# Optimization experiments

Measured on AMD Instinct MI355X. Metric: run time of the kernel, lower is better.

The kernel has to match this reference:

```python
import jax, jax.numpy as jnp
import numpy as np

N_NODES = 50000
N_EDGES = 800000
IN_CH = 128
OUT_CH = 64
HEADS = 2
NEG_SLOPE = 0.2


def _gat_conv(x, src, dst, W, a_src, a_dst, b, n):
    """PyG-style GATConv (eval mode: no dropout), self-loops already appended.
    x: [n, F_in]; W: [F_in, H*C]; a_src/a_dst: [H, C]; b: [H*C]."""
    H, C = a_src.shape
    h = (x @ W).reshape(n, H, C)                       # [n, H, C]
    alpha_src = jnp.sum(h * a_src, axis=-1)            # [n, H]
    alpha_dst = jnp.sum(h * a_dst, axis=-1)            # [n, H]
    e = alpha_src[src] + alpha_dst[dst]                # [E, H]
    e = jnp.where(e > 0, e, NEG_SLOPE * e)             # LeakyReLU(0.2)
    # neighbor-wise (destination-grouped) softmax, numerically stable
    m = jax.ops.segment_max(e, dst, num_segments=n)
    e = jnp.exp(e - m[dst])
    denom = jax.ops.segment_sum(e, dst, num_segments=n)
    alpha = e / (denom[dst] + 1e-16)                   # [E, H]
    out = jax.ops.segment_sum(alpha[:, :, None] * h[src], dst, num_segments=n)
    return out.reshape(n, H * C) + b


def setup_inputs() -> dict:
    key = jax.random.key(0)
    ks = jax.random.split(key, 12)
    s = 0.08  # glorot-ish scale
    x = jax.random.normal(ks[0], (N_NODES, IN_CH), dtype=jnp.float32)
    edge_index = jax.random.randint(ks[1], (2, N_EDGES), 0, N_NODES, dtype=jnp.int64)
    H, O = HEADS, OUT_CH
    return {
        "x": x,
        "edge_index": edge_index,
        "W1": jax.random.normal(ks[2], (IN_CH, H * 2 * O), dtype=jnp.float32) * s,
        "a_src1": jax.random.normal(ks[3], (H, 2 * O), dtype=jnp.float32) * s,
        "a_dst1": jax.random.normal(ks[4], (H, 2 * O), dtype=jnp.float32) * s,
        "b1": jnp.zeros((H * 2 * O,), dtype=jnp.float32),
        "W_mu": jax.random.normal(ks[5], (2 * O * H, H * O), dtype=jnp.float32) * s,
        "a_src_mu": jax.random.normal(ks[6], (H, O), dtype=jnp.float32) * s,
        "a_dst_mu": jax.random.normal(ks[7], (H, O), dtype=jnp.float32) * s,
        "b_mu": jnp.zeros((H * O,), dtype=jnp.float32),
        "W_ls": jax.random.normal(ks[8], (2 * O * H, H * O), dtype=jnp.float32) * s,
        "a_src_ls": jax.random.normal(ks[9], (H, O), dtype=jnp.float32) * s,
        "a_dst_ls": jax.random.normal(ks[10], (H, O), dtype=jnp.float32) * s,
        "b_ls": jnp.zeros((H * O,), dtype=jnp.float32),
    }


def reference(x, edge_index, W1, a_src1, a_dst1, b1,
              W_mu, a_src_mu, a_dst_mu, b_mu,
              W_ls, a_src_ls, a_dst_ls, b_ls):
    n = x.shape[0]
    loop = jnp.arange(n, dtype=edge_index.dtype)
    src = jnp.concatenate([edge_index[0], loop])  # PyG add_self_loops=True
    dst = jnp.concatenate([edge_index[1], loop])
    x1 = jax.nn.elu(_gat_conv(x, src, dst, W1, a_src1, a_dst1, b1, n))
    mu = _gat_conv(x1, src, dst, W_mu, a_src_mu, a_dst_mu, b_mu, n)
    logstd = _gat_conv(x1, src, dst, W_ls, a_src_ls, a_dst_ls, b_ls, n)
    return (mu, logstd)
```

## Files before the change

### kernel.cpp

```cpp
#include <hip/hip_runtime.h>


typedef unsigned short u16;
typedef unsigned int u32;
typedef _Float16 f16;
typedef f16 f16x8 __attribute__((ext_vector_type(8)));
typedef float f32x4v __attribute__((ext_vector_type(4)));

__device__ __forceinline__ u16 f2h(float f) {
    union { f16 h; u16 u; } t;
    t.h = (f16)f;
    return t.u;
}
__device__ __forceinline__ float4 loadh4(const u16* __restrict__ p, size_t i) {
    union { uint2 u; f16 h[4]; } t;
    t.u = *(const uint2*)(p + i);
    return make_float4((float)t.h[0], (float)t.h[1], (float)t.h[2], (float)t.h[3]);
}
__device__ __forceinline__ void store4(float* __restrict__ p, size_t i, float4 v) {
    *(float4*)(p + i) = v;
}
__device__ __forceinline__ void store4(u16* __restrict__ p, size_t i, float4 v) {
    union { uint2 u; f16 h[4]; } t;
    t.h[0] = (f16)v.x; t.h[1] = (f16)v.y; t.h[2] = (f16)v.z; t.h[3] = (f16)v.w;
    *(uint2*)(p + i) = t.u;
}

__global__ __launch_bounds__(256) void k_detect(const u32* __restrict__ ebuf,
                                                int* __restrict__ flag) {
    __shared__ int nz;
    if (threadIdx.x == 0) nz = 0;
    __syncthreads();
    if (ebuf[2 * threadIdx.x + 1] != 0u) atomicAdd(&nz, 1);
    __syncthreads();
    if (threadIdx.x == 0) *flag = (nz == 0) ? 1 : 0;
}

__global__ __launch_bounds__(256) void k_extract(const u32* __restrict__ ebuf, int E,
                                                 const int* __restrict__ flag,
                                                 int* __restrict__ se,
                                                 int* __restrict__ de,
                                                 int* __restrict__ deg) {
    int e = blockIdx.x * 256 + threadIdx.x;
    if (e >= E) return;
    int s, d;
    if (*flag) {
        s = (int)ebuf[2 * (size_t)e];
        d = (int)ebuf[2 * ((size_t)E + (size_t)e)];
    } else {
        s = (int)ebuf[e];
        d = (int)ebuf[(size_t)E + (size_t)e];
    }
    se[e] = s;
    de[e] = d;
    atomicAdd(&deg[d], 1);
}

__global__ __launch_bounds__(256) void k_scan_a(const int* __restrict__ deg, int n,
                                                int* __restrict__ bsum) {
    __shared__ int s[256];
    int i = blockIdx.x * 256 + threadIdx.x;
    s[threadIdx.x] = (i < n) ? deg[i] : 0;
    __syncthreads();
    for (int st = 128; st > 0; st >>= 1) {
        if (threadIdx.x < st) s[threadIdx.x] += s[threadIdx.x + st];
        __syncthreads();
    }
    if (threadIdx.x == 0) bsum[blockIdx.x] = s[0];
}

__global__ __launch_bounds__(256) void k_scan_b(int* __restrict__ bsum, int nb) {
    __shared__ int s[256];
    int t = threadIdx.x;
    int v = (t < nb) ? bsum[t] : 0;
    s[t] = v;
    __syncthreads();
    for (int off = 1; off < 256; off <<= 1) {
        int add = (t >= off) ? s[t - off] : 0;
        __syncthreads();
        s[t] += add;
        __syncthreads();
    }
    if (t < nb) bsum[t] = s[t] - v;
}

__global__ __launch_bounds__(256) void k_scan_c(const int* __restrict__ deg, int n,
                                                const int* __restrict__ bsum,
                                                int* __restrict__ rowptr,
                                                int* __restrict__ cursor, int E) {
    __shared__ int s[256];
    int t = threadIdx.x;
    int i = blockIdx.x * 256 + t;
    int v = (i < n) ? deg[i] : 0;
    s[t] = v;
    __syncthreads();
    for (int off = 1; off < 256; off <<= 1) {
        int add = (t >= off) ? s[t - off] : 0;
        __syncthreads();
        s[t] += add;
        __syncthreads();
    }
    if (i < n) {
        int ex = bsum[blockIdx.x] + s[t] - v;
        rowptr[i] = ex;
        cursor[i] = ex;
    }
    if (i == 0) rowptr[n] = E;
}

__global__ __launch_bounds__(256) void k_fill(const int* __restrict__ src,
                                              const int* __restrict__ dst, int E,
                                              int* __restrict__ cursor,
                                              int* __restrict__ csr_src) {
    int e = blockIdx.x * 256 + threadIdx.x;
    if (e < E) {
        int d = dst[e];
        int slot = atomicAdd(&cursor[d], 1);
        csr_src[slot] = src[e];
    }
}

__global__ __launch_bounds__(256) void k_cvt(const float* __restrict__ in,
                                             u16* __restrict__ out, int nElem) {
    int i = (blockIdx.x * 256 + threadIdx.x) * 4;
    if (i >= nElem) return;
    float4 v = *(const float4*)(in + i);
    store4(out, i, v);
}

__global__ __launch_bounds__(256) void k_tw(const float* __restrict__ Wl,
                                            const float* __restrict__ Wr, int split,
                                            int K, u16* __restrict__ Wt) {
    int idx = blockIdx.x * 256 + threadIdx.x;
    if (idx >= 256 * K) return;
    int c = idx / K, k = idx - c * K;
    float v;
    if (split == 256)
        v = Wl[(size_t)k * 256 + c];
    else
        v = (c < 128) ? Wl[(size_t)k * 128 + c] : Wr[(size_t)k * 128 + (c - 128)];
    Wt[idx] = f2h(v);
}

template <int K, int ALOGW>
__global__ __launch_bounds__(256) void k_gemm_mfma(
    const u16* __restrict__ Ah, const u16* __restrict__ Wt, u16* __restrict__ out,
    float* __restrict__ as_out, float* __restrict__ ad_out,
    const float* __restrict__ alo, const float* __restrict__ ahi,
    const float* __restrict__ dlo, const float* __restrict__ dhi, int M) {
    __shared__ u16 Bs[256 * 40];
    const int tid = threadIdx.x;
    const int wave = tid >> 6;
    const int lane = tid & 63;
    const int li = lane & 15;
    const int quad = lane >> 4;
    const int r0 = blockIdx.x * 64 + wave * 16;
    int arowi = r0 + li;
    if (arowi >= M) arowi = M - 1;
    const u16* arow = Ah + (size_t)arowi * K + quad * 8;

    f32x4v acc[16];
#pragma unroll
    for (int ct = 0; ct < 16; ct++) acc[ct] = (f32x4v)(0.f);

    for (int t = 0; t < K; t += 32) {
        __syncthreads();
        {
            const u16* src = Wt + (size_t)tid * K + t;
            u16* dst = Bs + tid * 40;
            uint4 v0 = ((const uint4*)src)[0];
            uint4 v1 = ((const uint4*)src)[1];
            uint4 v2 = ((const uint4*)src)[2];
            uint4 v3 = ((const uint4*)src)[3];
            ((uint4*)dst)[0] = v0;
            ((uint4*)(dst + 8))[0] = v1;
            ((uint4*)(dst + 16))[0] = v2;
            ((uint4*)(dst + 24))[0] = v3;
        }
        __syncthreads();
        f16x8 a = *(const f16x8*)(arow + t);
#pragma unroll
        for (int ct = 0; ct < 16; ct++) {
            f16x8 b = *(const f16x8*)(Bs + (ct * 16 + li) * 40 + quad * 8);
            acc[ct] = __builtin_amdgcn_mfma_f32_16x16x32_f16(a, b, acc[ct], 0, 0, 0);
        }
    }

#pragma unroll
    for (int reg = 0; reg < 4; reg++) {
        int grow = r0 + quad * 4 + reg;
        if (grow < M) {
            u16* orow = out + (size_t)grow * 256 + li;
#pragma unroll
            for (int ct = 0; ct < 16; ct++) orow[ct * 16] = f2h(acc[ct][reg]);
        }
    }

    const int NS = 64 >> ALOGW;
    const int SH = ALOGW - 2;
    float aw[16], dw[16];
#pragma unroll
    for (int ct = 0; ct < 16; ct++) {
        int col = ct * 16 + li;
        aw[ct] = (col < 128) ? alo[col] : ahi[col - 128];
        dw[ct] = (col < 128) ? dlo[col] : dhi[col - 128];
    }
#pragma unroll
    for (int reg = 0; reg < 4; reg++) {
        float s[4] = {0.f, 0.f, 0.f, 0.f};
        float d[4] = {0.f, 0.f, 0.f, 0.f};
#pragma unroll
        for (int ct = 0; ct < 16; ct++) {
            int sl = ct >> SH;
            s[sl] += acc[ct][reg] * aw[ct];
            d[sl] += acc[ct][reg] * dw[ct];
        }
#pragma unroll
        for (int sl = 0; sl < NS; sl++) {
#pragma unroll
            for (int m = 1; m <= 8; m <<= 1) {
                s[sl] += __shfl_xor(s[sl], m, 64);
                d[sl] += __shfl_xor(d[sl], m, 64);
            }
        }
        int grow = r0 + quad * 4 + reg;
        if (li == 0 && grow < M) {
#pragma unroll
            for (int sl = 0; sl < NS; sl++) {
                as_out[(size_t)grow * NS + sl] = s[sl];
                ad_out[(size_t)grow * NS + sl] = d[sl];
            }
        }
    }
}

template <int LOGW, int MODE, typename OT>
__global__ __launch_bounds__(256) void k_agg3(const u16* __restrict__ h,
                                              const int* __restrict__ rowptr,
                                              const int* __restrict__ csr_src,
                                              const float* __restrict__ as,
                                              const float* __restrict__ ad,
                                              const float* __restrict__ b_lo,
                                              const float* __restrict__ b_hi,
                                              OT* __restrict__ outp, int n,
                                              int nGrp) {
    const int NS = 64 >> LOGW;
    const int bid = blockIdx.x;
    const int xcd = bid & 7;
    const int half = xcd >> 2;
    const int grp = (bid >> 3) * 4 + (xcd & 3);
    if (grp >= nGrp) return;
    const int lane = threadIdx.x & 63;
    const int sub = lane >> 5;
    const int sl = lane & 31;
    const int wid0 = grp * 8 + (threadIdx.x >> 6) * 2 + sub;
    const bool ok = wid0 < n;
    const int wid = ok ? wid0 : (n - 1);
    const int col = half * 128 + sl * 4;
    const int slot = col >> (LOGW + 2);

    float adv = ad[(size_t)wid * NS + slot];
    float e = as[(size_t)wid * NS + slot] + adv;
    e = fmaxf(e, 0.2f * e);
    float w = __expf(e);
    float denom = w;
    float4 hv = loadh4(h, (size_t)wid * 256 + col);
    float acc0 = w * hv.x, acc1 = w * hv.y, acc2 = w * hv.z, acc3 = w * hv.w;

    int rb = 0, re = 0;
    if (ok) { rb = rowptr[wid0]; re = rowptr[wid0 + 1]; }
    int p = rb;
    for (; p + 4 <= re; p += 4) {
        int s0 = csr_src[p], s1 = csr_src[p + 1];
        int s2 = csr_src[p + 2], s3 = csr_src[p + 3];
        float e0 = as[(size_t)s0 * NS + slot] + adv;
        float e1 = as[(size_t)s1 * NS + slot] + adv;
        float e2 = as[(size_t)s2 * NS + slot] + adv;
        float e3 = as[(size_t)s3 * NS + slot] + adv;
        e0 = fmaxf(e0, 0.2f * e0);
        e1 = fmaxf(e1, 0.2f * e1);
        e2 = fmaxf(e2, 0.2f * e2);
        e3 = fmaxf(e3, 0.2f * e3);
        float w0 = __expf(e0), w1 = __expf(e1), w2 = __expf(e2), w3 = __expf(e3);
        float4 h0 = loadh4(h, (size_t)s0 * 256 + col);
        float4 h1 = loadh4(h, (size_t)s1 * 256 + col);
        float4 h2 = loadh4(h, (size_t)s2 * 256 + col);
        float4 h3 = loadh4(h, (size_t)s3 * 256 + col);
        denom += (w0 + w1) + (w2 + w3);
        acc0 += w0 * h0.x + w1 * h1.x + w2 * h2.x + w3 * h3.x;
        acc1 += w0 * h0.y + w1 * h1.y + w2 * h2.y + w3 * h3.y;
        acc2 += w0 * h0.z + w1 * h1.z + w2 * h2.z + w3 * h3.z;
        acc3 += w0 * h0.w + w1 * h1.w + w2 * h2.w + w3 * h3.w;
    }
    for (; p < re; ++p) {
        int s = csr_src[p];
        float ev = as[(size_t)s * NS + slot] + adv;
        ev = fmaxf(ev, 0.2f * ev);
        float ww = __expf(ev);
        denom += ww;
        float4 hh = loadh4(h, (size_t)s * 256 + col);
        acc0 += ww * hh.x;
        acc1 += ww * hh.y;
        acc2 += ww * hh.z;
        acc3 += ww * hh.w;
    }
    float inv = 1.0f / (denom + 1e-16f);

    const float* bp = half ? b_hi : b_lo;
    const int ci = sl * 4;
    float4 bv = *(const float4*)(bp + ci);
    float v0 = acc0 * inv + bv.x;
    float v1 = acc1 * inv + bv.y;
    float v2 = acc2 * inv + bv.z;
    float v3 = acc3 * inv + bv.w;

    if (!ok) return;
    if (MODE == 0) {
        v0 = v0 > 0.f ? v0 : expm1f(v0);
        v1 = v1 > 0.f ? v1 : expm1f(v1);
        v2 = v2 > 0.f ? v2 : expm1f(v2);
        v3 = v3 > 0.f ? v3 : expm1f(v3);
        store4((u16*)outp, (size_t)wid0 * 256 + col, make_float4(v0, v1, v2, v3));
    } else {
        size_t base = half ? ((size_t)n * 128 + (size_t)wid0 * 128 + ci)
                           : ((size_t)wid0 * 128 + ci);
        store4((float*)outp, base, make_float4(v0, v1, v2, v3));
    }
}

extern "C" void kernel_launch(void* const* d_in, const int* in_sizes, int n_in,
                              void* d_out, int out_size, void* d_ws, size_t ws_size,
                              hipStream_t stream) {
    const float* x = (const float*)d_in[0];
    const u32* ebuf = (const u32*)d_in[1];
    const float* W1 = (const float*)d_in[2];
    const float* a_src1 = (const float*)d_in[3];
    const float* a_dst1 = (const float*)d_in[4];
    const float* b1 = (const float*)d_in[5];
    const float* W_mu = (const float*)d_in[6];
    const float* a_src_mu = (const float*)d_in[7];
    const float* a_dst_mu = (const float*)d_in[8];
    const float* b_mu = (const float*)d_in[9];
    const float* W_ls = (const float*)d_in[10];
    const float* a_src_ls = (const float*)d_in[11];
    const float* a_dst_ls = (const float*)d_in[12];
    const float* b_ls = (const float*)d_in[13];

    const int n = in_sizes[0] / 128;
    const int E = in_sizes[1] / 2;

    char* base = (char*)d_ws;
    size_t off = 0;
    auto alloc = [&](size_t b) -> char* {
        char* p = base + off;
        off = (off + b + 255) & ~(size_t)255;
        return p;
    };
    int* rowptr = (int*)alloc((size_t)(n + 1) * 4);
    int* cursor = (int*)alloc((size_t)n * 4);
    int* csr = (int*)alloc((size_t)E * 4);
    int* bsum = (int*)alloc(256 * 4);
    int* eflag = (int*)alloc(256);
    int* se = (int*)alloc((size_t)E * 4);
    int* de = (int*)alloc((size_t)E * 4);
    float* as = (float*)alloc((size_t)n * 4 * 4);
    float* ad = (float*)alloc((size_t)n * 4 * 4);
    u16* W1t = (u16*)alloc(256 * 128 * 2);
    u16* Wt2 = (u16*)alloc(256 * 256 * 2);
    u16* x1h = (u16*)alloc((size_t)n * 256 * 2);
    u16* xh = x1h;
    u16* h = (u16*)alloc((size_t)n * 256 * 2);

    const int nb = (n + 255) / 256;
    const int eg = (E + 255) / 256;
    const int gg = (n + 63) / 64;
    const int nGrp = (n + 7) / 8;
    const int aggGrid = 8 * ((nGrp + 3) / 4);

    hipMemsetAsync(cursor, 0, (size_t)n * 4, stream);
    k_detect<<<1, 256, 0, stream>>>(ebuf, eflag);
    k_extract<<<eg, 256, 0, stream>>>(ebuf, E, eflag, se, de, cursor);
    k_scan_a<<<nb, 256, 0, stream>>>(cursor, n, bsum);
    k_scan_b<<<1, 256, 0, stream>>>(bsum, nb);
    k_scan_c<<<nb, 256, 0, stream>>>(cursor, n, bsum, rowptr, cursor, E);
    k_fill<<<eg, 256, 0, stream>>>(se, de, E, cursor, csr);

    k_cvt<<<(n * 128 / 4 + 255) / 256, 256, 0, stream>>>(x, xh, n * 128);
    k_tw<<<(256 * 128 + 255) / 256, 256, 0, stream>>>(W1, W1, 256, 128, W1t);
    k_tw<<<(256 * 256 + 255) / 256, 256, 0, stream>>>(W_mu, W_ls, 128, 256, Wt2);

    k_gemm_mfma<128, 5><<<gg, 256, 0, stream>>>(xh, W1t, h, as, ad, a_src1,
                                                a_src1 + 128, a_dst1, a_dst1 + 128,
                                                n);
    k_agg3<5, 0, u16><<<aggGrid, 256, 0, stream>>>(h, rowptr, csr, as, ad, b1,
                                                   b1 + 128, x1h, n, nGrp);

    k_gemm_mfma<256, 4><<<gg, 256, 0, stream>>>(x1h, Wt2, h, as, ad, a_src_mu,
                                                a_src_ls, a_dst_mu, a_dst_ls, n);
    k_agg3<4, 1, float><<<aggGrid, 256, 0, stream>>>(h, rowptr, csr, as, ad, b_mu,
                                                     b_ls, (float*)d_out, n, nGrp);
}
```

Measured before the change: 388.1 us.

## Precompute per-edge softmax weights in CSR order before aggregation

A destination array is now written alongside the CSR source array. A new per-edge kernel computes exp(LeakyReLU(a_src+a_dst)) for each head slot into a slot-major weight buffer. The aggregation kernel then reads these weights with contiguous vector loads instead of gathering a_src per neighbour and recomputing exp. The inner loop is also unrolled to 8 edges using int4/float4 loads of indices and weights. This costs an extra kernel launch, an extra pass over the edges and more workspace. The vector loads start at arbitrary row offsets, so they may be misaligned.

```diff
diff --git a/kernel.cpp b/kernel.cpp
--- a/kernel.cpp
+++ b/kernel.cpp
@@ -111,12 +111,14 @@
 __global__ __launch_bounds__(256) void k_fill(const int* __restrict__ src,
                                               const int* __restrict__ dst, int E,
                                               int* __restrict__ cursor,
-                                              int* __restrict__ csr_src) {
+                                              int* __restrict__ csr_src,
+                                              int* __restrict__ csr_dst) {
     int e = blockIdx.x * 256 + threadIdx.x;
     if (e < E) {
         int d = dst[e];
         int slot = atomicAdd(&cursor[d], 1);
         csr_src[slot] = src[e];
+        csr_dst[slot] = d;
     }
 }
 
@@ -140,6 +142,38 @@
     else
         v = (c < 128) ? Wl[(size_t)k * 128 + c] : Wr[(size_t)k * 128 + (c - 128)];
     Wt[idx] = f2h(v);
+}
+
+template <int NS>
+__global__ __launch_bounds__(256) void k_w(const int* __restrict__ csr_src,
+                                           const int* __restrict__ csr_dst,
+                                           const float* __restrict__ as,
+                                           const float* __restrict__ ad,
+                                           float* __restrict__ wp, int E) {
+    int i = blockIdx.x * 256 + threadIdx.x;
+    if (i >= E) return;
+    int s = csr_src[i], d = csr_dst[i];
+    if (NS == 2) {
+        float2 a = *(const float2*)(as + (size_t)s * 2);
+        float2 b = *(const float2*)(ad + (size_t)d * 2);
+        float e0 = a.x + b.x, e1 = a.y + b.y;
+        e0 = fmaxf(e0, 0.2f * e0);
+        e1 = fmaxf(e1, 0.2f * e1);
+        wp[i] = __expf(e0);
+        wp[(size_t)E + i] = __expf(e1);
+    } else {
+        float4 a = *(const float4*)(as + (size_t)s * 4);
+        float4 b = *(const float4*)(ad + (size_t)d * 4);
+        float e0 = a.x + b.x, e1 = a.y + b.y, e2 = a.z + b.z, e3 = a.w + b.w;
+        e0 = fmaxf(e0, 0.2f * e0);
+        e1 = fmaxf(e1, 0.2f * e1);
+        e2 = fmaxf(e2, 0.2f * e2);
+        e3 = fmaxf(e3, 0.2f * e3);
+        wp[i] = __expf(e0);
+        wp[(size_t)E + i] = __expf(e1);
+        wp[2 * (size_t)E + i] = __expf(e2);
+        wp[3 * (size_t)E + i] = __expf(e3);
+    }
 }
 
 template <int K, int ALOGW>
@@ -235,15 +269,12 @@
 }
 
 template <int LOGW, int MODE, typename OT>
-__global__ __launch_bounds__(256) void k_agg3(const u16* __restrict__ h,
-                                              const int* __restrict__ rowptr,
-                                              const int* __restrict__ csr_src,
-                                              const float* __restrict__ as,
-                                              const float* __restrict__ ad,
-                                              const float* __restrict__ b_lo,
-                                              const float* __restrict__ b_hi,
-                                              OT* __restrict__ outp, int n,
-                                              int nGrp) {
+__global__ __launch_bounds__(256) void k_agg4(
+    const u16* __restrict__ h, const int* __restrict__ rowptr,
+    const int* __restrict__ csr_src, const float* __restrict__ wp,
+    const float* __restrict__ as, const float* __restrict__ ad,
+    const float* __restrict__ b_lo, const float* __restrict__ b_hi,
+    OT* __restrict__ outp, int n, int nGrp, int E) {
     const int NS = 64 >> LOGW;
     const int bid = blockIdx.x;
     const int xcd = bid & 7;
@@ -258,9 +289,9 @@
     const int wid = ok ? wid0 : (n - 1);
     const int col = half * 128 + sl * 4;
     const int slot = col >> (LOGW + 2);
-
-    float adv = ad[(size_t)wid * NS + slot];
-    float e = as[(size_t)wid * NS + slot] + adv;
+    const float* __restrict__ wpl = wp + (size_t)slot * E;
+
+    float e = as[(size_t)wid * NS + slot] + ad[(size_t)wid * NS + slot];
     e = fmaxf(e, 0.2f * e);
     float w = __expf(e);
     float denom = w;
@@ -270,35 +301,47 @@
     int rb = 0, re = 0;
     if (ok) { rb = rowptr[wid0]; re = rowptr[wid0 + 1]; }
     int p = rb;
+    for (; p + 8 <= re; p += 8) {
+        int4 sA = *(const int4*)(csr_src + p);
+        int4 sB = *(const int4*)(csr_src + p + 4);
+        float4 wA = *(const float4*)(wpl + p);
+        float4 wB = *(const float4*)(wpl + p + 4);
+        float4 h0 = loadh4(h, (size_t)sA.x * 256 + col);
+        float4 h1 = loadh4(h, (size_t)sA.y * 256 + col);
+        float4 h2 = loadh4(h, (size_t)sA.z * 256 + col);
+        float4 h3 = loadh4(h, (size_t)sA.w * 256 + col);
+        float4 h4 = loadh4(h, (size_t)sB.x * 256 + col);
+        float4 h5 = loadh4(h, (size_t)sB.y * 256 + col);
+        float4 h6 = loadh4(h, (size_t)sB.z * 256 + col);
+        float4 h7 = loadh4(h, (size_t)sB.w * 256 + col);
+        denom += (wA.x + wA.y + wA.z + wA.w) + (wB.x + wB.y + wB.z + wB.w);
+        acc0 += wA.x * h0.x + wA.y * h1.x + wA.z * h2.x + wA.w * h3.x +
+                wB.x * h4.x + wB.y * h5.x + wB.z * h6.x + wB.w * h7.x;
+        acc1 += wA.x * h0.y + wA.y * h1.y + wA.z * h2.y + wA.w * h3.y +
+                wB.x * h4.y + wB.y * h5.y + wB.z * h6.y + wB.w * h7.y;
+        acc2 += wA.x * h0.z + wA.y * h1.z + wA.z * h2.z + wA.w * h3.z +
+                wB.x * h4.z + wB.y * h5.z + wB.z * h6.z + wB.w * h7.z;
+        acc3 += wA.x * h0.w + wA.y * h1.w + wA.z * h2.w + wA.w * h3.w +
+                wB.x * h4.w + wB.y * h5.w + wB.z * h6.w + wB.w * h7.w;
+    }
     for (; p + 4 <= re; p += 4) {
-        int s0 = csr_src[p], s1 = csr_src[p + 1];
-        int s2 = csr_src[p + 2], s3 = csr_src[p + 3];
-        float e0 = as[(size_t)s0 * NS + slot] + adv;
-        float e1 = as[(size_t)s1 * NS + slot] + adv;
-        float e2 = as[(size_t)s2 * NS + slot] + adv;
-        float e3 = as[(size_t)s3 * NS + slot] + adv;
-        e0 = fmaxf(e0, 0.2f * e0);
-        e1 = fmaxf(e1, 0.2f * e1);
-        e2 = fmaxf(e2, 0.2f * e2);
-        e3 = fmaxf(e3, 0.2f * e3);
-        float w0 = __expf(e0), w1 = __expf(e1), w2 = __expf(e2), w3 = __expf(e3);
-        float4 h0 = loadh4(h, (size_t)s0 * 256 + col);
-        float4 h1 = loadh4(h, (size_t)s1 * 256 + col);
-        float4 h2 = loadh4(h, (size_t)s2 * 256 + col);
-        float4 h3 = loadh4(h, (size_t)s3 * 256 + col);
-        denom += (w0 + w1) + (w2 + w3);
-        acc0 += w0 * h0.x + w1 * h1.x + w2 * h2.x + w3 * h3.x;
-        acc1 += w0 * h0.y + w1 * h1.y + w2 * h2.y + w3 * h3.y;
-        acc2 += w0 * h0.z + w1 * h1.z + w2 * h2.z + w3 * h3.z;
-        acc3 += w0 * h0.w + w1 * h1.w + w2 * h2.w + w3 * h3.w;
+        int4 sA = *(const int4*)(csr_src + p);
+        float4 wA = *(const float4*)(wpl + p);
+        float4 h0 = loadh4(h, (size_t)sA.x * 256 + col);
+        float4 h1 = loadh4(h, (size_t)sA.y * 256 + col);
+        float4 h2 = loadh4(h, (size_t)sA.z * 256 + col);
+        float4 h3 = loadh4(h, (size_t)sA.w * 256 + col);
+        denom += (wA.x + wA.y) + (wA.z + wA.w);
+        acc0 += wA.x * h0.x + wA.y * h1.x + wA.z * h2.x + wA.w * h3.x;
+        acc1 += wA.x * h0.y + wA.y * h1.y + wA.z * h2.y + wA.w * h3.y;
+        acc2 += wA.x * h0.z + wA.y * h1.z + wA.z * h2.z + wA.w * h3.z;
+        acc3 += wA.x * h0.w + wA.y * h1.w + wA.z * h2.w + wA.w * h3.w;
     }
     for (; p < re; ++p) {
         int s = csr_src[p];
-        float ev = as[(size_t)s * NS + slot] + adv;
-        ev = fmaxf(ev, 0.2f * ev);
-        float ww = __expf(ev);
+        float ww = wpl[p];
+        float4 hh = loadh4(h, (size_t)s * 256 + col);
         denom += ww;
-        float4 hh = loadh4(h, (size_t)s * 256 + col);
         acc0 += ww * hh.x;
         acc1 += ww * hh.y;
         acc2 += ww * hh.z;
@@ -359,12 +402,14 @@
     int* rowptr = (int*)alloc((size_t)(n + 1) * 4);
     int* cursor = (int*)alloc((size_t)n * 4);
     int* csr = (int*)alloc((size_t)E * 4);
+    int* csrd = (int*)alloc((size_t)E * 4);
     int* bsum = (int*)alloc(256 * 4);
     int* eflag = (int*)alloc(256);
     int* se = (int*)alloc((size_t)E * 4);
     int* de = (int*)alloc((size_t)E * 4);
     float* as = (float*)alloc((size_t)n * 4 * 4);
     float* ad = (float*)alloc((size_t)n * 4 * 4);
+    float* wp = (float*)alloc((size_t)E * 4 * 4);
     u16* W1t = (u16*)alloc(256 * 128 * 2);
     u16* Wt2 = (u16*)alloc(256 * 256 * 2);
     u16* x1h = (u16*)alloc((size_t)n * 256 * 2);
@@ -383,7 +428,7 @@
     k_scan_a<<<nb, 256, 0, stream>>>(cursor, n, bsum);
     k_scan_b<<<1, 256, 0, stream>>>(bsum, nb);
     k_scan_c<<<nb, 256, 0, stream>>>(cursor, n, bsum, rowptr, cursor, E);
-    k_fill<<<eg, 256, 0, stream>>>(se, de, E, cursor, csr);
+    k_fill<<<eg, 256, 0, stream>>>(se, de, E, cursor, csr, csrd);
 
     k_cvt<<<(n * 128 / 4 + 255) / 256, 256, 0, stream>>>(x, xh, n * 128);
     k_tw<<<(256 * 128 + 255) / 256, 256, 0, stream>>>(W1, W1, 256, 128, W1t);
@@ -392,11 +437,14 @@
     k_gemm_mfma<128, 5><<<gg, 256, 0, stream>>>(xh, W1t, h, as, ad, a_src1,
                                                 a_src1 + 128, a_dst1, a_dst1 + 128,
                                                 n);
-    k_agg3<5, 0, u16><<<aggGrid, 256, 0, stream>>>(h, rowptr, csr, as, ad, b1,
-                                                   b1 + 128, x1h, n, nGrp);
+    k_w<2><<<eg, 256, 0, stream>>>(csr, csrd, as, ad, wp, E);
+    k_agg4<5, 0, u16><<<aggGrid, 256, 0, stream>>>(h, rowptr, csr, wp, as, ad, b1,
+                                                   b1 + 128, x1h, n, nGrp, E);
 
     k_gemm_mfma<256, 4><<<gg, 256, 0, stream>>>(x1h, Wt2, h, as, ad, a_src_mu,
                                                 a_src_ls, a_dst_mu, a_dst_ls, n);
-    k_agg3<4, 1, float><<<aggGrid, 256, 0, stream>>>(h, rowptr, csr, as, ad, b_mu,
-                                                     b_ls, (float*)d_out, n, nGrp);
-}
+    k_w<4><<<eg, 256, 0, stream>>>(csr, csrd, as, ad, wp, E);
+    k_agg4<4, 1, float><<<aggGrid, 256, 0, stream>>>(h, rowptr, csr, wp, as, ad,
+                                                     b_mu, b_ls, (float*)d_out, n,
+                                                     nGrp, E);
+}
```

Result: no change. 391.8 us (+1.0%).
